# Performance work log

Hardware: AMD Instinct MI355X
Metric: run time of the kernel (lower is better)

## Reference

```python
import jax, jax.numpy as jnp
import numpy as np

RADIUS = 0.2
NSAMPLE = 32
USE_XYZ = True

B, N, S, C = 8, 8192, 2048, 64


def setup_inputs() -> dict:
    key = jax.random.key(0)
    k1, k2, k3 = jax.random.split(key, 3)
    xyz = jax.random.uniform(k1, (B, N, 3), dtype=jnp.float32)
    new_xyz = jax.random.uniform(k2, (B, S, 3), dtype=jnp.float32)
    features = jax.random.normal(k3, (B, N, C), dtype=jnp.float32)
    return {"xyz": xyz, "new_xyz": new_xyz, "features": features}


def _ball_query(new_xyz, xyz, radius, nsample):
    # new_xyz: (B,S,3), xyz: (B,N,3) -> idx (B,S,nsample) int32
    n = xyz.shape[1]
    d2 = jnp.sum((new_xyz[:, :, None, :] - xyz[:, None, :, :]) ** 2, axis=-1)  # (B,S,N)
    mask = d2 < radius * radius
    # keys: index j if inside ball else N (sentinel); smallest nsample keys = first
    # nsample in-ball indices in ascending j order (matches CUDA ball_query order).
    keys = jnp.where(mask, jnp.arange(n, dtype=jnp.int32), jnp.int32(n))
    neg_vals, _ = jax.lax.top_k(-keys, nsample)  # top_k of -keys -> smallest keys
    idx = -neg_vals  # (B,S,nsample), ascending
    first = idx[..., 0:1]
    idx = jnp.where(idx == n, first, idx)   # pad empty slots with first hit
    idx = jnp.where(idx == n, 0, idx)       # balls with zero hits -> index 0
    return idx


def _group(points, idx):
    # points: (B,N,D), idx: (B,S,K) -> (B,S,K,D)
    return jax.vmap(lambda p, i: p[i])(points, idx)


def reference(xyz, new_xyz, features):
    idx = _ball_query(new_xyz, xyz, RADIUS, NSAMPLE)
    grouped_xyz = _group(xyz, idx) - new_xyz[:, :, None, :]  # (B,S,K,3)
    grouped_feat = _group(features, idx)                      # (B,S,K,C)
    if USE_XYZ:
        new_features = jnp.concatenate([grouped_xyz, grouped_feat], axis=-1)
    else:
        new_features = grouped_feat
    return jnp.transpose(new_features, (0, 3, 1, 2))  # (B, C+3, S, K)
```

## Files before the change

### kernel.cpp

```cpp
#include <hip/hip_runtime.h>

#define BB 8
#define NN 8192
#define SS 2048
#define CC 64
#define NS 32
#define COUT 67

__global__ __launch_bounds__(256) void scan_kernel(
    const float* __restrict__ xyz,
    const float* __restrict__ new_xyz,
    int* __restrict__ idx_ws)
{
#pragma clang fp contract(off)
    const int wave = threadIdx.x >> 6;
    const int lane = threadIdx.x & 63;
    const int qid  = blockIdx.x * 4 + wave;
    const int b = qid >> 11;
    const int s = qid & 2047;

    const float R2 = 0.04f;

    const float* ctr = new_xyz + ((size_t)b * SS + s) * 3;
    const float cx = ctr[0], cy = ctr[1], cz = ctr[2];
    const float* xb = xyz + (size_t)b * NN * 3;

    int* myidx = idx_ws + (size_t)qid * NS;
    const unsigned long long lt = (1ull << lane) - 1ull;

    int total = 0;
    int firstIdx = -1;
    for (int j0 = 0; j0 < NN && total < NS; j0 += 256) {
        float d2v[4];
#pragma unroll
        for (int u = 0; u < 4; ++u) {
            const int j = j0 + u * 64 + lane;
            const float* p = xb + (size_t)j * 3;
            const float dx = p[0] - cx;
            const float dy = p[1] - cy;
            const float dz = p[2] - cz;
            float d2 = dx * dx;
            d2 = d2 + dy * dy;
            d2 = d2 + dz * dz;
            d2v[u] = d2;
        }
#pragma unroll
        for (int u = 0; u < 4; ++u) {
            const bool hit = d2v[u] < R2;
            const unsigned long long mask = __ballot(hit);
            if (firstIdx < 0 && mask != 0ull)
                firstIdx = j0 + u * 64 + __builtin_ctzll(mask);
            if (hit) {
                const int pos = total + __popcll(mask & lt);
                if (pos < NS) myidx[pos] = j0 + u * 64 + lane;
            }
            total += __popcll(mask);
        }
    }
    if (total < NS) {
        const int fill = (total > 0) ? firstIdx : 0;
        if (lane >= total && lane < NS) myidx[lane] = fill;
    }
}

__global__ __launch_bounds__(256) void gather_kernel(
    const float* __restrict__ xyz,
    const float* __restrict__ new_xyz,
    const float* __restrict__ feat,
    const int* __restrict__ idx_ws,
    float* __restrict__ out)
{
#pragma clang fp contract(off)
    const int wave = threadIdx.x >> 6;
    const int lane = threadIdx.x & 63;
    const int qid  = blockIdx.x * 4 + wave;
    const int b = qid >> 11;
    const int s = qid & 2047;

    const int k = lane & 31;
    const int h = lane >> 5;

    const int ik = idx_ws[(size_t)qid * NS + k];

    const float* ctr = new_xyz + ((size_t)b * SS + s) * 3;
    const float cx = ctr[0], cy = ctr[1], cz = ctr[2];
    const float* xb = xyz + (size_t)b * NN * 3;

    const size_t plane = (size_t)SS * NS;

    if (h == 0) {
        const float* p = xb + (size_t)ik * 3;
        const size_t ob = (((size_t)b * COUT + 0) * SS + s) * NS + k;
        out[ob]             = p[0] - cx;
        out[ob + plane]     = p[1] - cy;
        out[ob + 2 * plane] = p[2] - cz;
    }

    const float* frow = feat + ((size_t)b * NN + ik) * CC;
    const size_t obase = (((size_t)b * COUT + 3) * SS + s) * NS + k;
    for (int cf = 0; cf < CC; cf += 8) {
        const int c0 = cf + 4 * h;
        const float4 f = *(const float4*)(frow + c0);
        const size_t o = obase + (size_t)c0 * plane;
        out[o]             = f.x;
        out[o + plane]     = f.y;
        out[o + 2 * plane] = f.z;
        out[o + 3 * plane] = f.w;
    }
}

extern "C" void kernel_launch(void* const* d_in, const int* in_sizes, int n_in,
                              void* d_out, int out_size, void* d_ws, size_t ws_size,
                              hipStream_t stream) {
    const float* xyz     = (const float*)d_in[0];
    const float* new_xyz = (const float*)d_in[1];
    const float* feat    = (const float*)d_in[2];
    float* out = (float*)d_out;
    int* idx_ws = (int*)d_ws;

    scan_kernel<<<dim3((BB * SS) / 4), dim3(256), 0, stream>>>(xyz, new_xyz, idx_ws);
    gather_kernel<<<dim3((BB * SS) / 4), dim3(256), 0, stream>>>(xyz, new_xyz, feat, idx_ws, out);
}
```

Baseline: 196.0 us.

## Write grouped xyz in scan kernel and retile feature gather per channel-quad

The scan kernel now writes the relative xyz offsets straight into the output as it finds hits, so the gather kernel no longer reloads xyz and centers. The gather kernel is reorganized: each block stages 128 queries' indices in shared memory and handles one group of 4 channels. Consecutive threads then write contiguous output positions within each channel plane, giving coalesced stores in place of the earlier 32-wide strided pattern. The cost is that the same feature rows are gathered by 16 separate blocks, and the scan kernel takes on extra scattered stores.

Measured after the change: 211.5 us. 1.08x slower.

```diff
diff --git a/kernel.cpp b/kernel.cpp
--- a/kernel.cpp
+++ b/kernel.cpp
@@ -10,7 +10,8 @@
 __global__ __launch_bounds__(256) void scan_kernel(
     const float* __restrict__ xyz,
     const float* __restrict__ new_xyz,
-    int* __restrict__ idx_ws)
+    int* __restrict__ idx_ws,
+    float* __restrict__ out)
 {
 #pragma clang fp contract(off)
     const int wave = threadIdx.x >> 6;
@@ -28,84 +29,86 @@
     int* myidx = idx_ws + (size_t)qid * NS;
     const unsigned long long lt = (1ull << lane) - 1ull;
 
+    const size_t plane = (size_t)SS * NS;
+    float* oxyz = out + (size_t)b * COUT * plane + (size_t)s * NS;
+
     int total = 0;
     int firstIdx = -1;
     for (int j0 = 0; j0 < NN && total < NS; j0 += 256) {
-        float d2v[4];
+        float dxv[4], dyv[4], dzv[4];
 #pragma unroll
         for (int u = 0; u < 4; ++u) {
             const int j = j0 + u * 64 + lane;
             const float* p = xb + (size_t)j * 3;
-            const float dx = p[0] - cx;
-            const float dy = p[1] - cy;
-            const float dz = p[2] - cz;
-            float d2 = dx * dx;
-            d2 = d2 + dy * dy;
-            d2 = d2 + dz * dz;
-            d2v[u] = d2;
+            dxv[u] = p[0] - cx;
+            dyv[u] = p[1] - cy;
+            dzv[u] = p[2] - cz;
         }
 #pragma unroll
         for (int u = 0; u < 4; ++u) {
-            const bool hit = d2v[u] < R2;
+            float d2 = dxv[u] * dxv[u];
+            d2 = d2 + dyv[u] * dyv[u];
+            d2 = d2 + dzv[u] * dzv[u];
+            const bool hit = d2 < R2;
             const unsigned long long mask = __ballot(hit);
             if (firstIdx < 0 && mask != 0ull)
                 firstIdx = j0 + u * 64 + __builtin_ctzll(mask);
             if (hit) {
                 const int pos = total + __popcll(mask & lt);
-                if (pos < NS) myidx[pos] = j0 + u * 64 + lane;
+                if (pos < NS) {
+                    myidx[pos] = j0 + u * 64 + lane;
+                    oxyz[pos]             = dxv[u];
+                    oxyz[plane + pos]     = dyv[u];
+                    oxyz[2 * plane + pos] = dzv[u];
+                }
             }
             total += __popcll(mask);
         }
     }
-    if (total < NS) {
+    if (total < NS && lane >= total && lane < NS) {
         const int fill = (total > 0) ? firstIdx : 0;
-        if (lane >= total && lane < NS) myidx[lane] = fill;
+        myidx[lane] = fill;
+        const float* p = xb + (size_t)fill * 3;
+        oxyz[lane]             = p[0] - cx;
+        oxyz[plane + lane]     = p[1] - cy;
+        oxyz[2 * plane + lane] = p[2] - cz;
     }
 }
 
 __global__ __launch_bounds__(256) void gather_kernel(
-    const float* __restrict__ xyz,
-    const float* __restrict__ new_xyz,
     const float* __restrict__ feat,
     const int* __restrict__ idx_ws,
     float* __restrict__ out)
 {
-#pragma clang fp contract(off)
-    const int wave = threadIdx.x >> 6;
-    const int lane = threadIdx.x & 63;
-    const int qid  = blockIdx.x * 4 + wave;
-    const int b = qid >> 11;
-    const int s = qid & 2047;
+    __shared__ int idx_sh[128 * NS];
+    const int t = threadIdx.x;
+    const int sTile = blockIdx.x;
+    const int cq    = blockIdx.y;
+    const int b     = blockIdx.z;
 
-    const int k = lane & 31;
-    const int h = lane >> 5;
-
-    const int ik = idx_ws[(size_t)qid * NS + k];
-
-    const float* ctr = new_xyz + ((size_t)b * SS + s) * 3;
-    const float cx = ctr[0], cy = ctr[1], cz = ctr[2];
-    const float* xb = xyz + (size_t)b * NN * 3;
+    const int qbase = (b << 11) + (sTile << 7);
+    const int4* src = (const int4*)(idx_ws + (size_t)qbase * NS);
+    int4* dst = (int4*)idx_sh;
+#pragma unroll
+    for (int i = 0; i < 4; ++i)
+        dst[t + 256 * i] = src[t + 256 * i];
+    __syncthreads();
 
     const size_t plane = (size_t)SS * NS;
+    const int c0 = 3 + cq * 4;
+    const float* fb = feat + (size_t)b * NN * CC + cq * 4;
+    float* ob = out + ((size_t)b * COUT + c0) * plane + (size_t)(sTile << 7) * NS;
 
-    if (h == 0) {
-        const float* p = xb + (size_t)ik * 3;
-        const size_t ob = (((size_t)b * COUT + 0) * SS + s) * NS + k;
-        out[ob]             = p[0] - cx;
-        out[ob + plane]     = p[1] - cy;
-        out[ob + 2 * plane] = p[2] - cz;
-    }
-
-    const float* frow = feat + ((size_t)b * NN + ik) * CC;
-    const size_t obase = (((size_t)b * COUT + 3) * SS + s) * NS + k;
-    for (int cf = 0; cf < CC; cf += 8) {
-        const int c0 = cf + 4 * h;
-        const float4 f = *(const float4*)(frow + c0);
-        const size_t o = obase + (size_t)c0 * plane;
-        out[o]             = f.x;
-        out[o + plane]     = f.y;
-        out[o + 2 * plane] = f.z;
-        out[o + 3 * plane] = f.w;
+#pragma unroll 4
+    for (int i = 0; i < 16; ++i) {
+        const int p = t + (i << 8);
+        const int row = idx_sh[p];
+        const float4 f = *(const float4*)(fb + (size_t)row * CC);
+        float* o = ob + p;
+        o[0]         = f.x;
+        o[plane]     = f.y;
+        o[2 * plane] = f.z;
+        o[3 * plane] = f.w;
     }
 }
 
@@ -118,6 +121,6 @@
     float* out = (float*)d_out;
     int* idx_ws = (int*)d_ws;
 
-    scan_kernel<<<dim3((BB * SS) / 4), dim3(256), 0, stream>>>(xyz, new_xyz, idx_ws);
-    gather_kernel<<<dim3((BB * SS) / 4), dim3(256), 0, stream>>>(xyz, new_xyz, feat, idx_ws, out);
+    scan_kernel<<<dim3((BB * SS) / 4), dim3(256), 0, stream>>>(xyz, new_xyz, idx_ws, out);
+    gather_kernel<<<dim3(16, 16, BB), dim3(256), 0, stream>>>(feat, idx_ws, out);
 }
```

## Stage gathered features in LDS to emit wide coalesced output stores

Applied to the files above, without the earlier changes.

Restructures the gather kernel so each block handles 8 queries and one half of the channels, first writing gathered xyz offsets and features into a channel-major shared-memory tile, then storing each channel plane as contiguous 1KB float4 writes. This aims to replace many narrow 128-byte scalar stores per channel with wide coalesced stores to the large transposed output. It adds shared memory use, two barriers, and an idle wave for some iterations in the store loop.

New measurement: 195.8 us. No clear change (-0.1%).

```diff
diff --git a/kernel.cpp b/kernel.cpp
--- a/kernel.cpp
+++ b/kernel.cpp
@@ -6,6 +6,8 @@
 #define CC 64
 #define NS 32
 #define COUT 67
+#define QT 8
+#define PMAX 35
 
 __global__ __launch_bounds__(256) void scan_kernel(
     const float* __restrict__ xyz,
@@ -71,41 +73,63 @@
     float* __restrict__ out)
 {
 #pragma clang fp contract(off)
-    const int wave = threadIdx.x >> 6;
-    const int lane = threadIdx.x & 63;
-    const int qid  = blockIdx.x * 4 + wave;
-    const int b = qid >> 11;
-    const int s = qid & 2047;
+    __shared__ float tile[PMAX * QT * NS];
+    __shared__ int idx_sh[QT * NS];
 
-    const int k = lane & 31;
-    const int h = lane >> 5;
+    const int t     = threadIdx.x;
+    const int sTile = blockIdx.x;
+    const int half  = blockIdx.y;
+    const int b     = blockIdx.z;
 
-    const int ik = idx_ws[(size_t)qid * NS + k];
+    const int s0 = sTile * QT;
+    const int qbase = (b << 11) + s0;
 
-    const float* ctr = new_xyz + ((size_t)b * SS + s) * 3;
-    const float cx = ctr[0], cy = ctr[1], cz = ctr[2];
-    const float* xb = xyz + (size_t)b * NN * 3;
+    idx_sh[t] = idx_ws[(size_t)qbase * NS + t];
+    __syncthreads();
 
+    const int q = t >> 5;
+    const int row = idx_sh[t];
+
+    const float* frow = feat + ((size_t)b * NN + row) * CC + half * 32;
+    if (half == 0) {
+        const float* ctr = new_xyz + ((size_t)b * SS + s0 + q) * 3;
+        const float* p   = xyz + ((size_t)b * NN + row) * 3;
+        tile[0 * 256 + t] = p[0] - ctr[0];
+        tile[1 * 256 + t] = p[1] - ctr[1];
+        tile[2 * 256 + t] = p[2] - ctr[2];
+#pragma unroll
+        for (int i = 0; i < 8; ++i) {
+            const float4 f = *(const float4*)(frow + i * 4);
+            tile[(3 + i * 4 + 0) * 256 + t] = f.x;
+            tile[(3 + i * 4 + 1) * 256 + t] = f.y;
+            tile[(3 + i * 4 + 2) * 256 + t] = f.z;
+            tile[(3 + i * 4 + 3) * 256 + t] = f.w;
+        }
+    } else {
+#pragma unroll
+        for (int i = 0; i < 8; ++i) {
+            const float4 f = *(const float4*)(frow + i * 4);
+            tile[(i * 4 + 0) * 256 + t] = f.x;
+            tile[(i * 4 + 1) * 256 + t] = f.y;
+            tile[(i * 4 + 2) * 256 + t] = f.z;
+            tile[(i * 4 + 3) * 256 + t] = f.w;
+        }
+    }
+    __syncthreads();
+
+    const int P     = half ? 32 : PMAX;
+    const int cbase = half ? PMAX : 0;
+    const int wv = t >> 6;
+    const int ln = t & 63;
     const size_t plane = (size_t)SS * NS;
-
-    if (h == 0) {
-        const float* p = xb + (size_t)ik * 3;
-        const size_t ob = (((size_t)b * COUT + 0) * SS + s) * NS + k;
-        out[ob]             = p[0] - cx;
-        out[ob + plane]     = p[1] - cy;
-        out[ob + 2 * plane] = p[2] - cz;
-    }
-
-    const float* frow = feat + ((size_t)b * NN + ik) * CC;
-    const size_t obase = (((size_t)b * COUT + 3) * SS + s) * NS + k;
-    for (int cf = 0; cf < CC; cf += 8) {
-        const int c0 = cf + 4 * h;
-        const float4 f = *(const float4*)(frow + c0);
-        const size_t o = obase + (size_t)c0 * plane;
-        out[o]             = f.x;
-        out[o + plane]     = f.y;
-        out[o + 2 * plane] = f.z;
-        out[o + 3 * plane] = f.w;
+    float* ob = out + (((size_t)b * COUT + cbase) * SS + s0) * NS;
+#pragma unroll
+    for (int i = 0; i < 9; ++i) {
+        const int p = i * 4 + wv;
+        if (p < P) {
+            const float4 v = *(const float4*)(tile + p * 256 + ln * 4);
+            *(float4*)(ob + (size_t)p * plane + ln * 4) = v;
+        }
     }
 }
 
@@ -119,5 +143,5 @@
     int* idx_ws = (int*)d_ws;
 
     scan_kernel<<<dim3((BB * SS) / 4), dim3(256), 0, stream>>>(xyz, new_xyz, idx_ws);
-    gather_kernel<<<dim3((BB * SS) / 4), dim3(256), 0, stream>>>(xyz, new_xyz, feat, idx_ws, out);
+    gather_kernel<<<dim3(SS / QT, 2, BB), dim3(256), 0, stream>>>(xyz, new_xyz, feat, idx_ws, out);
 }
```
